# Performance work log

Measured on AMD Instinct MI355X. Metric: run time of the kernel, lower is better.

## Reference

```python
import jax, jax.numpy as jnp
import numpy as np

NUM_HEADS = 16

def setup_inputs() -> dict:
    key = jax.random.key(0)
    ks = jax.random.split(key, 6)
    b, t, d = 2, 2048, 1024
    s = 0.02
    return {
        "x": jax.random.normal(ks[0], (b, t, d), jnp.float32),
        "Wq": jax.random.normal(ks[1], (d, d), jnp.float32) * s,
        "Wk": jax.random.normal(ks[2], (d, d), jnp.float32) * s,
        "Wv": jax.random.normal(ks[3], (d, d), jnp.float32) * s,
        "Wo": jax.random.normal(ks[4], (d, d), jnp.float32) * s,
        "bo": jnp.zeros((d,), jnp.float32),
    }

def reference(x, Wq, Wk, Wv, Wo, bo):
    b, t, d = x.shape
    h = NUM_HEADS
    hd = d // h  # head_dim = d_out / num_heads
    # torch nn.Linear: y = x @ W.T (qkv_bias=False)
    def split_heads(y):
        return y.reshape(b, t, h, hd).transpose(0, 2, 1, 3)  # [b,h,t,hd]
    q = split_heads(x @ Wq.T)
    k = split_heads(x @ Wk.T)
    v = split_heads(x @ Wv.T)
    scale = 1.0 / jnp.sqrt(jnp.asarray(hd, x.dtype))
    # NOTE: original forward computes but never applies the causal mask or dropout
    scores = jnp.einsum('bhqd,bhkd->bhqk', q, k) * scale
    attn = jax.nn.softmax(scores, axis=-1)
    ctx = jnp.einsum('bhqk,bhkd->bhqd', attn, v)
    ctx = ctx.transpose(0, 2, 1, 3).reshape(b, t, d)
    return ctx @ Wo.T + bo
```

## Files before the change

### kernel.cpp

```cpp
#include <hip/hip_runtime.h>
#include <hip/hip_bf16.h>
#include <math.h>
#include <stdint.h>
#include <string.h>

#define TSEQ 2048
#define DMODEL 1024
#define NH 16
#define HD 64
#define BROWS 4096
#define BH 32

typedef __attribute__((ext_vector_type(8))) short short8;
typedef __attribute__((ext_vector_type(4))) float floatx4;
typedef __attribute__((ext_vector_type(16))) float floatx16;

#define MFMA16 __builtin_amdgcn_mfma_f32_16x16x32_bf16
#define MFMA32 __builtin_amdgcn_mfma_f32_32x32x16_bf16
#define SWZ8(r, q) ((((q) ^ ((r) & 7)) * 8))

#define QSCALE 0.18033688011112042f

__device__ __forceinline__ unsigned short bf16_rne(float f) {
    uint32_t u = __float_as_uint(f);
    u += 0x7FFFu + ((u >> 16) & 1u);
    return (unsigned short)(u >> 16);
}

__device__ __forceinline__ uint32_t pack_bf16x2(float a, float b) {
    __hip_bfloat162 h = __float22bfloat162_rn(float2{a, b});
    uint32_t r;
    memcpy(&r, &h, 4);
    return r;
}

__device__ __forceinline__ void split_bf16(float f, short& hi, short& lo) {
    uint32_t u = __float_as_uint(f);
    hi = (short)(u >> 16);
    float hif = __uint_as_float(u & 0xFFFF0000u);
    lo = (short)bf16_rne(f - hif);
}

__device__ __forceinline__ void async16(const void* g, void* l) {
    __builtin_amdgcn_global_load_lds(
        (__attribute__((address_space(1))) const uint32_t*)g,
        (__attribute__((address_space(3))) uint32_t*)l, 16, 0, 0);
}

struct PackArgs {
    const float4* x;
    ushort4* xb;
    const float4* w[3];
    ushort4* wb[3];
    const float4* wo;
    ushort4* woh;
    ushort4* wol;
};
__global__ __launch_bounds__(256) void pack_all(PackArgs a) {
    const int y = blockIdx.y;
    const int base = blockIdx.x * 256 + threadIdx.x;
    if (y == 0) {
#pragma unroll
        for (int it = 0; it < 4; ++it) {
            int i = base + it * 262144;
            float4 f = a.x[i];
            a.xb[i] = make_ushort4(bf16_rne(f.x), bf16_rne(f.y),
                                   bf16_rne(f.z), bf16_rne(f.w));
        }
    } else if (y <= 3) {
        int w = y - 1;
        float4 f = a.w[w][base];
        a.wb[w][base] = make_ushort4(bf16_rne(f.x), bf16_rne(f.y),
                                     bf16_rne(f.z), bf16_rne(f.w));
    } else {
        float4 f = a.wo[base];
        short h0, l0, h1, l1, h2, l2, h3, l3;
        split_bf16(f.x, h0, l0); split_bf16(f.y, h1, l1);
        split_bf16(f.z, h2, l2); split_bf16(f.w, h3, l3);
        a.woh[base] = make_ushort4(h0, h1, h2, h3);
        a.wol[base] = make_ushort4(l0, l1, l2, l3);
    }
}

__global__ __launch_bounds__(256) void gemm_qkv(
    const short* __restrict__ Xb,
    const short* __restrict__ Bq, const short* __restrict__ Bk,
    const short* __restrict__ Bv,
    short* __restrict__ Qo, short* __restrict__ Ko, short* __restrict__ Vo) {
    __shared__ short sA[128 * 64];
    __shared__ short sB[128 * 64];
    const int K = DMODEL;

    const int tid = threadIdx.x;
    const int lane = tid & 63, wave = tid >> 6;
    const int quad = lane >> 4, col = lane & 15;
    const int m0 = blockIdx.y * 128, n0 = blockIdx.x * 128;
    const int which = n0 >> 10;
    const int nn0 = n0 & 1023;
    const int wm = wave >> 1, wn = wave & 1;

    const short* B = (which == 0) ? Bq : (which == 1) ? Bk : Bv;
    const short* Asrc = Xb + (size_t)m0 * K;
    const short* Bsrc = B + (size_t)nn0 * K;

    const int srow = lane >> 3;
    const int soff = (((lane & 7) ^ srow) * 8);

    floatx4 acc[4][4] = {};

    for (int k0 = 0; k0 < K; k0 += 64) {
        __syncthreads();
#pragma unroll
        for (int j = 0; j < 8; ++j) {
            int idx = wave * 8 + j;
            int sub = idx & 15;
            const short* s = (idx < 16) ? Asrc : Bsrc;
            short* d = (idx < 16) ? sA : sB;
            async16(s + (size_t)(sub * 8 + srow) * K + k0 + soff, d + sub * 512);
        }
        __syncthreads();

#pragma unroll
        for (int s2 = 0; s2 < 2; ++s2) {
            short8 a_b[4], b_b[4];
#pragma unroll
            for (int mi = 0; mi < 4; ++mi) {
                int r = wm * 64 + mi * 16 + col;
                a_b[mi] = *(const short8*)&sA[r * 64 + SWZ8(r, s2 * 4 + quad)];
            }
#pragma unroll
            for (int ni = 0; ni < 4; ++ni) {
                int r = wn * 64 + ni * 16 + col;
                b_b[ni] = *(const short8*)&sB[r * 64 + SWZ8(r, s2 * 4 + quad)];
            }
            if (which == 2) {
#pragma unroll
                for (int mi = 0; mi < 4; ++mi)
#pragma unroll
                    for (int ni = 0; ni < 4; ++ni)
                        acc[mi][ni] = MFMA16(a_b[mi], b_b[ni], acc[mi][ni], 0, 0, 0);
            } else {
#pragma unroll
                for (int mi = 0; mi < 4; ++mi)
#pragma unroll
                    for (int ni = 0; ni < 4; ++ni)
                        acc[mi][ni] = MFMA16(b_b[ni], a_b[mi], acc[mi][ni], 0, 0, 0);
            }
        }
    }

    const int mb = m0 + wm * 64;
    const int nlb = nn0 + wn * 64;
    if (which == 2) {
#pragma unroll
        for (int ni = 0; ni < 4; ++ni) {
            int n = nlb + ni * 16 + col;
            int h = n >> 6, hd = n & 63;
#pragma unroll
            for (int mi = 0; mi < 4; ++mi) {
                int m4 = mb + mi * 16 + quad * 4;
                int b = m4 >> 11, t0 = m4 & 2047;
                int sw = (t0 & 0x33) | ((t0 & 4) << 1) | ((t0 & 8) >> 1);
                int tsw = (t0 & ~63) | ((((sw >> 3) ^ (hd & 7)) << 3) | (sw & 7));
                size_t row = ((size_t)(b * NH + h) * HD + hd) * TSEQ;
                *(ushort4*)&Vo[row + tsw] =
                    make_ushort4(bf16_rne(acc[mi][ni][0]), bf16_rne(acc[mi][ni][1]),
                                 bf16_rne(acc[mi][ni][2]), bf16_rne(acc[mi][ni][3]));
            }
        }
    } else {
        short* O = (which == 0) ? Qo : Ko;
        const float sc = (which == 0) ? QSCALE : 1.0f;
#pragma unroll
        for (int mi = 0; mi < 4; ++mi) {
            int m = mb + mi * 16 + col;
            int b = m >> 11, t = m & 2047;
#pragma unroll
            for (int ni = 0; ni < 4; ++ni) {
                int n = nlb + ni * 16 + quad * 4;
                int h = n >> 6, hd = n & 63;
                int hds = (which == 1) ? ((((hd >> 3) ^ (t & 7)) << 3) | (hd & 7)) : hd;
                size_t idx = ((size_t)(b * NH + h) * TSEQ + t) * HD + hds;
                *(ushort4*)&O[idx] =
                    make_ushort4(bf16_rne(acc[mi][ni][0] * sc), bf16_rne(acc[mi][ni][1] * sc),
                                 bf16_rne(acc[mi][ni][2] * sc), bf16_rne(acc[mi][ni][3] * sc));
            }
        }
    }
}

#define ATTN_COMPUTE(DB)                                                        \
    {                                                                           \
        floatx16 s[4] = {};                                                     \
        __builtin_amdgcn_s_setprio(1);                                          \
        _Pragma("unroll")                                                       \
        for (int u = 0; u < 2; ++u)                                             \
            _Pragma("unroll")                                                   \
            for (int mm = 0; mm < 2; ++mm)                                      \
                _Pragma("unroll")                                               \
                for (int ks = 0; ks < 4; ++ks) {                                \
                    short8 kf = *(const short8*)(kB[ks] + (DB) * 8192 + u * 4096 + mm * 2048); \
                    s[u * 2 + mm] = MFMA32(kf, qf[ks], s[u * 2 + mm], 0, 0, 0); \
                }                                                               \
        __builtin_amdgcn_s_setprio(0);                                          \
        _Pragma("unroll")                                                       \
        for (int m = 0; m < 4; ++m) {                                           \
            float p[16];                                                        \
            _Pragma("unroll")                                                   \
            for (int r = 0; r < 16; ++r) {                                      \
                p[r] = __builtin_amdgcn_exp2f(s[m][r]);                         \
                lv[r & 3] += p[r];                                              \
            }                                                                   \
            _Pragma("unroll")                                                   \
            for (int c = 0; c < 2; ++c) {                                       \
                union { short8 v; uint32_t w[4]; } pf;                          \
                pf.w[0] = pack_bf16x2(p[8 * c + 0], p[8 * c + 1]);              \
                pf.w[1] = pack_bf16x2(p[8 * c + 2], p[8 * c + 3]);              \
                pf.w[2] = pack_bf16x2(p[8 * c + 4], p[8 * c + 5]);              \
                pf.w[3] = pack_bf16x2(p[8 * c + 6], p[8 * c + 7]);              \
                const int t = m * 2 + c, uu = t >> 2, tt = t & 3;               \
                __builtin_amdgcn_s_setprio(1);                                  \
                _Pragma("unroll")                                               \
                for (int mi = 0; mi < 2; ++mi) {                                \
                    short8 vf = *(const short8*)(vB[tt] + (DB) * 8192 + uu * 4096 + mi * 2048); \
                    O2[mi] = MFMA32(vf, pf.v, O2[mi], 0, 0, 0);                 \
                }                                                               \
                __builtin_amdgcn_s_setprio(0);                                  \
            }                                                                   \
        }                                                                       \
    }

#define STAGE(LB)                                                               \
    {                                                                           \
        _Pragma("unroll")                                                       \
        for (int j = 0; j < 8; ++j)                                             \
            async16(gb + (size_t)j * gstride, (LB) + j * 512);                  \
        gb += ktstep;                                                           \
    }

__global__ __launch_bounds__(256, 2) void attn_bf16(
    const short* __restrict__ Qb, const short* __restrict__ Kb,
    const short* __restrict__ Vb, short* __restrict__ Cb) {
    __shared__ short sK[2][2][64 * 64];
    __shared__ short sV[2][2][64 * 64];

    const int tid = threadIdx.x;
    const int lane = tid & 63, wave = tid >> 6;
    const int q5 = lane & 31, hh = lane >> 5, l7 = lane & 7;
    const int qt = blockIdx.x, bh = blockIdx.y;
    const size_t bhoff = (size_t)bh * TSEQ * HD;

    const size_t qrow = (size_t)(qt * 128 + wave * 32 + q5) * HD;
    short8 qf[4];
#pragma unroll
    for (int ks = 0; ks < 4; ++ks)
        qf[ks] = *(const short8*)&Qb[bhoff + qrow + ks * 16 + hh * 8];

    const int srow = lane >> 3, schunk = (lane & 7) * 8;
    const int isV = wave >> 1, tl = wave & 1;
    const short* gb;
    size_t gstride, ktstep;
    if (!isV) {
        gb = Kb + bhoff + (size_t)(tl * 64 + srow) * HD + schunk;
        gstride = (size_t)8 * HD;
        ktstep = (size_t)128 * HD;
    } else {
        gb = Vb + bhoff + (size_t)srow * TSEQ + tl * 64 + schunk;
        gstride = (size_t)8 * TSEQ;
        ktstep = 128;
    }
    short* lb0 = isV ? sV[0][tl] : sK[0][tl];
    short* lb1 = isV ? sV[1][tl] : sK[1][tl];

    const short* kB[4];
    const short* vB[4];
#pragma unroll
    for (int w = 0; w < 4; ++w) {
        kB[w] = &sK[0][0][q5 * 64 + (((2 * w + hh) ^ l7) * 8)];
        vB[w] = &sV[0][0][q5 * 64 + (((2 * w + hh) ^ l7) * 8)];
    }

    floatx4 lv = {};
    floatx16 O2[2] = {};

    STAGE(lb0);

    for (int kt2 = 0; kt2 < 8; ++kt2) {
        STAGE(lb1);
        asm volatile("s_waitcnt vmcnt(8)" ::: "memory");
        __builtin_amdgcn_s_barrier();
        ATTN_COMPUTE(0);
        __builtin_amdgcn_s_barrier();

        if (kt2 < 7) {
            STAGE(lb0);
            asm volatile("s_waitcnt vmcnt(8)" ::: "memory");
        } else {
            asm volatile("s_waitcnt vmcnt(0)" ::: "memory");
        }
        __builtin_amdgcn_s_barrier();
        ATTN_COMPUTE(1);
        __builtin_amdgcn_s_barrier();
    }

    float l_r = (lv[0] + lv[1]) + (lv[2] + lv[3]);
    l_r += __shfl_xor(l_r, 32);
    const float inv = 1.0f / l_r;

    const int b = bh >> 4, h = bh & 15;
    const int trow = qt * 128 + wave * 32 + q5;
    const size_t obase = (size_t)(b * TSEQ + trow) * DMODEL + h * 64;
#pragma unroll
    for (int mi = 0; mi < 2; ++mi)
#pragma unroll
        for (int g = 0; g < 4; ++g) {
            uint2 pk;
            pk.x = pack_bf16x2(O2[mi][4 * g + 0] * inv, O2[mi][4 * g + 1] * inv);
            pk.y = pack_bf16x2(O2[mi][4 * g + 2] * inv, O2[mi][4 * g + 3] * inv);
            *(uint2*)&Cb[obase + mi * 32 + g * 8 + hh * 4] = pk;
        }
}

__global__ __launch_bounds__(256) void gemm_out(
    const short* __restrict__ Ab,
    const short* __restrict__ Bh, const short* __restrict__ Bl,
    const float* __restrict__ bias, float* __restrict__ Of) {
    __shared__ short sA[128 * 64];
    __shared__ short sBh[64 * 64];
    __shared__ short sBl[64 * 64];
    const int K = DMODEL, N = DMODEL;

    const int tid = threadIdx.x;
    const int lane = tid & 63, wave = tid >> 6;
    const int quad = lane >> 4, col = lane & 15;
    const int m0 = blockIdx.y * 128, n0 = blockIdx.x * 64;
    const int wm = wave >> 1, wn = wave & 1;

    const short* Asrc = Ab + (size_t)m0 * K;
    const short* Bhsrc = Bh + (size_t)n0 * K;
    const short* Blsrc = Bl + (size_t)n0 * K;
    const int srow = lane >> 3;
    const int soff = (((lane & 7) ^ srow) * 8);

    floatx4 acc[4][2] = {};

    for (int k0 = 0; k0 < K; k0 += 64) {
        __syncthreads();
#pragma unroll
        for (int j = 0; j < 8; ++j) {
            int idx = wave * 8 + j;
            int buf = (idx < 16) ? 0 : (idx < 24) ? 1 : 2;
            int sub = (buf == 0) ? idx : (buf == 1) ? idx - 16 : idx - 24;
            const short* s = (buf == 0) ? Asrc : (buf == 1) ? Bhsrc : Blsrc;
            short* d = (buf == 0) ? sA : (buf == 1) ? sBh : sBl;
            async16(s + (size_t)(sub * 8 + srow) * K + k0 + soff, d + sub * 512);
        }
        __syncthreads();

#pragma unroll
        for (int s2 = 0; s2 < 2; ++s2) {
            short8 a_b[4], b_h[2], b_l[2];
#pragma unroll
            for (int mi = 0; mi < 4; ++mi) {
                int r = wm * 64 + mi * 16 + col;
                a_b[mi] = *(const short8*)&sA[r * 64 + SWZ8(r, s2 * 4 + quad)];
            }
#pragma unroll
            for (int ni = 0; ni < 2; ++ni) {
                int r = wn * 32 + ni * 16 + col;
                b_h[ni] = *(const short8*)&sBh[r * 64 + SWZ8(r, s2 * 4 + quad)];
                b_l[ni] = *(const short8*)&sBl[r * 64 + SWZ8(r, s2 * 4 + quad)];
            }
#pragma unroll
            for (int mi = 0; mi < 4; ++mi)
#pragma unroll
                for (int ni = 0; ni < 2; ++ni) {
                    acc[mi][ni] = MFMA16(b_h[ni], a_b[mi], acc[mi][ni], 0, 0, 0);
                    acc[mi][ni] = MFMA16(b_l[ni], a_b[mi], acc[mi][ni], 0, 0, 0);
                }
        }
    }

    const int mb = m0 + wm * 64, nb = n0 + wn * 32;
#pragma unroll
    for (int mi = 0; mi < 4; ++mi) {
        int m = mb + mi * 16 + col;
#pragma unroll
        for (int ni = 0; ni < 2; ++ni) {
            int n = nb + ni * 16 + quad * 4;
            float4 bv = *(const float4*)&bias[n];
            float4 o = make_float4(acc[mi][ni][0] + bv.x, acc[mi][ni][1] + bv.y,
                                   acc[mi][ni][2] + bv.z, acc[mi][ni][3] + bv.w);
            *(float4*)&Of[(size_t)m * N + n] = o;
        }
    }
}

extern "C" void kernel_launch(void* const* d_in, const int* in_sizes, int n_in,
                              void* d_out, int out_size, void* d_ws, size_t ws_size,
                              hipStream_t stream) {
    const float* x  = (const float*)d_in[0];
    const float* Wq = (const float*)d_in[1];
    const float* Wk = (const float*)d_in[2];
    const float* Wv = (const float*)d_in[3];
    const float* Wo = (const float*)d_in[4];
    const float* bo = (const float*)d_in[5];
    float* out = (float*)d_out;

    const size_t NX = (size_t)BROWS * DMODEL;
    const size_t NW = (size_t)DMODEL * DMODEL;
    short* p = (short*)d_ws;
    short *xb = p;
    short *wqb = xb + NX;
    short *wkb = wqb + NW;
    short *wvb = wkb + NW;
    short *woh = wvb + NW; short *wol = woh + NW;
    short *qb = wol + NW;
    short *kb = qb + NX;
    short *vb = kb + NX;
    short *cb = vb + NX;

    PackArgs pa;
    pa.x = (const float4*)x; pa.xb = (ushort4*)xb;
    pa.w[0] = (const float4*)Wq; pa.wb[0] = (ushort4*)wqb;
    pa.w[1] = (const float4*)Wk; pa.wb[1] = (ushort4*)wkb;
    pa.w[2] = (const float4*)Wv; pa.wb[2] = (ushort4*)wvb;
    pa.wo = (const float4*)Wo; pa.woh = (ushort4*)woh; pa.wol = (ushort4*)wol;
    pack_all<<<dim3(1024, 5), dim3(256), 0, stream>>>(pa);

    gemm_qkv<<<dim3(3 * DMODEL / 128, BROWS / 128), dim3(256), 0, stream>>>(
        xb, wqb, wkb, wvb, qb, kb, vb);

    attn_bf16<<<dim3(TSEQ / 128, BH), dim3(256), 0, stream>>>(qb, kb, vb, cb);

    gemm_out<<<dim3(DMODEL / 64, BROWS / 128), dim3(256), 0, stream>>>(cb, woh, wol, bo, out);
}
```

Baseline: 192.8 us.

## Split attention KV sequence across two wave groups with LDS reduction

The attention kernel now runs 512 threads per block: two groups of four waves each take half of the key/value sequence for the same 128 query rows. Each group stages 64-key chunks into its own LDS buffers, and at the end the second group writes its partial O and row sums to shared memory for the first group to combine and normalise. This doubles the waves working on each query tile and halves the per-wave serial KV loop, aiming for more latency hiding. In exchange it adds a final LDS exchange and extra barriers, and needs more per-CU resources for the bigger blocks.

```diff
diff --git a/kernel.cpp b/kernel.cpp
--- a/kernel.cpp
+++ b/kernel.cpp
@@ -189,26 +189,24 @@
     }
 }
 
-#define ATTN_COMPUTE(DB)                                                        \
+#define ATTN_CHUNK(DB)                                                          \
     {                                                                           \
-        floatx16 s[4] = {};                                                     \
+        floatx16 s2[2] = {};                                                    \
         __builtin_amdgcn_s_setprio(1);                                          \
         _Pragma("unroll")                                                       \
-        for (int u = 0; u < 2; ++u)                                             \
+        for (int mm = 0; mm < 2; ++mm)                                          \
             _Pragma("unroll")                                                   \
-            for (int mm = 0; mm < 2; ++mm)                                      \
-                _Pragma("unroll")                                               \
-                for (int ks = 0; ks < 4; ++ks) {                                \
-                    short8 kf = *(const short8*)(kB[ks] + (DB) * 8192 + u * 4096 + mm * 2048); \
-                    s[u * 2 + mm] = MFMA32(kf, qf[ks], s[u * 2 + mm], 0, 0, 0); \
-                }                                                               \
+            for (int ks = 0; ks < 4; ++ks) {                                    \
+                short8 kf = *(const short8*)(kBp[ks] + (DB) * 4096 + mm * 2048);\
+                s2[mm] = MFMA32(kf, qf[ks], s2[mm], 0, 0, 0);                   \
+            }                                                                   \
         __builtin_amdgcn_s_setprio(0);                                          \
         _Pragma("unroll")                                                       \
-        for (int m = 0; m < 4; ++m) {                                           \
+        for (int mm = 0; mm < 2; ++mm) {                                        \
             float p[16];                                                        \
             _Pragma("unroll")                                                   \
             for (int r = 0; r < 16; ++r) {                                      \
-                p[r] = __builtin_amdgcn_exp2f(s[m][r]);                         \
+                p[r] = __builtin_amdgcn_exp2f(s2[mm][r]);                       \
                 lv[r & 3] += p[r];                                              \
             }                                                                   \
             _Pragma("unroll")                                                   \
@@ -218,11 +216,11 @@
                 pf.w[1] = pack_bf16x2(p[8 * c + 2], p[8 * c + 3]);              \
                 pf.w[2] = pack_bf16x2(p[8 * c + 4], p[8 * c + 5]);              \
                 pf.w[3] = pack_bf16x2(p[8 * c + 6], p[8 * c + 7]);              \
-                const int t = m * 2 + c, uu = t >> 2, tt = t & 3;               \
+                const int tt = mm * 2 + c;                                      \
                 __builtin_amdgcn_s_setprio(1);                                  \
                 _Pragma("unroll")                                               \
                 for (int mi = 0; mi < 2; ++mi) {                                \
-                    short8 vf = *(const short8*)(vB[tt] + (DB) * 8192 + uu * 4096 + mi * 2048); \
+                    short8 vf = *(const short8*)(vBp[tt] + (DB) * 4096 + mi * 2048); \
                     O2[mi] = MFMA32(vf, pf.v, O2[mi], 0, 0, 0);                 \
                 }                                                               \
                 __builtin_amdgcn_s_setprio(0);                                  \
@@ -232,52 +230,55 @@
 
 #define STAGE(LB)                                                               \
     {                                                                           \
-        _Pragma("unroll")                                                       \
-        for (int j = 0; j < 8; ++j)                                             \
-            async16(gb + (size_t)j * gstride, (LB) + j * 512);                  \
-        gb += ktstep;                                                           \
-    }
-
-__global__ __launch_bounds__(256, 2) void attn_bf16(
+        async16(gb + 0 * gj, (LB) + 0 * 512);                                   \
+        async16(gb + 1 * gj, (LB) + 1 * 512);                                   \
+        async16(gb + 2 * gj, (LB) + 2 * 512);                                   \
+        async16(gb + 3 * gj, (LB) + 3 * 512);                                   \
+        gb += cstep;                                                            \
+    }
+
+__global__ __launch_bounds__(512, 4) void attn_bf16(
     const short* __restrict__ Qb, const short* __restrict__ Kb,
     const short* __restrict__ Vb, short* __restrict__ Cb) {
-    __shared__ short sK[2][2][64 * 64];
-    __shared__ short sV[2][2][64 * 64];
+    __shared__ short sK[2][2][4096];
+    __shared__ short sV[2][2][4096];
 
     const int tid = threadIdx.x;
     const int lane = tid & 63, wave = tid >> 6;
     const int q5 = lane & 31, hh = lane >> 5, l7 = lane & 7;
+    const int qg = wave & 3;
+    const int st = wave >> 2;
     const int qt = blockIdx.x, bh = blockIdx.y;
     const size_t bhoff = (size_t)bh * TSEQ * HD;
 
-    const size_t qrow = (size_t)(qt * 128 + wave * 32 + q5) * HD;
+    const size_t qrow = (size_t)(qt * 128 + qg * 32 + q5) * HD;
     short8 qf[4];
 #pragma unroll
     for (int ks = 0; ks < 4; ++ks)
         qf[ks] = *(const short8*)&Qb[bhoff + qrow + ks * 16 + hh * 8];
 
     const int srow = lane >> 3, schunk = (lane & 7) * 8;
-    const int isV = wave >> 1, tl = wave & 1;
+    const int isV = qg >> 1, half = qg & 1;
     const short* gb;
-    size_t gstride, ktstep;
+    size_t gj, cstep;
     if (!isV) {
-        gb = Kb + bhoff + (size_t)(tl * 64 + srow) * HD + schunk;
-        gstride = (size_t)8 * HD;
-        ktstep = (size_t)128 * HD;
+        gb = Kb + bhoff + (size_t)(st * 1024 + half * 32 + srow) * HD + schunk;
+        gj = (size_t)8 * HD;
+        cstep = (size_t)64 * HD;
     } else {
-        gb = Vb + bhoff + (size_t)srow * TSEQ + tl * 64 + schunk;
-        gstride = (size_t)8 * TSEQ;
-        ktstep = 128;
-    }
-    short* lb0 = isV ? sV[0][tl] : sK[0][tl];
-    short* lb1 = isV ? sV[1][tl] : sK[1][tl];
-
-    const short* kB[4];
-    const short* vB[4];
+        gb = Vb + bhoff + (size_t)(half * 32 + srow) * TSEQ + st * 1024 + schunk;
+        gj = (size_t)8 * TSEQ;
+        cstep = 64;
+    }
+    short (*dst)[4096] = isV ? sV[st] : sK[st];
+    short* lb0 = dst[0] + half * 2048;
+    short* lb1 = dst[1] + half * 2048;
+
+    const short *kBp[4], *vBp[4];
 #pragma unroll
     for (int w = 0; w < 4; ++w) {
-        kB[w] = &sK[0][0][q5 * 64 + (((2 * w + hh) ^ l7) * 8)];
-        vB[w] = &sV[0][0][q5 * 64 + (((2 * w + hh) ^ l7) * 8)];
+        kBp[w] = &sK[st][0][q5 * 64 + (((2 * w + hh) ^ l7) * 8)];
+        vBp[w] = &sV[st][0][q5 * 64 + (((2 * w + hh) ^ l7) * 8)];
     }
 
     floatx4 lv = {};
@@ -285,40 +286,66 @@
 
     STAGE(lb0);
 
-    for (int kt2 = 0; kt2 < 8; ++kt2) {
+    for (int c2 = 0; c2 < 8; ++c2) {
         STAGE(lb1);
-        asm volatile("s_waitcnt vmcnt(8)" ::: "memory");
+        asm volatile("s_waitcnt vmcnt(4)" ::: "memory");
         __builtin_amdgcn_s_barrier();
-        ATTN_COMPUTE(0);
+        ATTN_CHUNK(0);
         __builtin_amdgcn_s_barrier();
 
-        if (kt2 < 7) {
+        if (c2 < 7) {
             STAGE(lb0);
-            asm volatile("s_waitcnt vmcnt(8)" ::: "memory");
+            asm volatile("s_waitcnt vmcnt(4)" ::: "memory");
         } else {
             asm volatile("s_waitcnt vmcnt(0)" ::: "memory");
         }
         __builtin_amdgcn_s_barrier();
-        ATTN_COMPUTE(1);
+        ATTN_CHUNK(1);
         __builtin_amdgcn_s_barrier();
     }
 
-    float l_r = (lv[0] + lv[1]) + (lv[2] + lv[3]);
-    l_r += __shfl_xor(l_r, 32);
-    const float inv = 1.0f / l_r;
-
-    const int b = bh >> 4, h = bh & 15;
-    const int trow = qt * 128 + wave * 32 + q5;
-    const size_t obase = (size_t)(b * TSEQ + trow) * DMODEL + h * 64;
-#pragma unroll
-    for (int mi = 0; mi < 2; ++mi)
-#pragma unroll
-        for (int g = 0; g < 4; ++g) {
+    float lp = (lv[0] + lv[1]) + (lv[2] + lv[3]);
+    float* xch = (float*)&sK[0][0][0];
+    float* xl  = (float*)&sV[0][0][0];
+    __syncthreads();
+    if (st == 1) {
+#pragma unroll
+        for (int j = 0; j < 8; ++j) {
+            float4 v = make_float4(O2[j >> 2][(j & 3) * 4 + 0],
+                                   O2[j >> 2][(j & 3) * 4 + 1],
+                                   O2[j >> 2][(j & 3) * 4 + 2],
+                                   O2[j >> 2][(j & 3) * 4 + 3]);
+            *(float4*)&xch[qg * 2048 + lane * 32 + ((j ^ l7) * 4)] = v;
+        }
+        xl[qg * 64 + lane] = lp;
+    }
+    __syncthreads();
+    if (st == 0) {
+        lp += xl[qg * 64 + lane];
+        lp += __shfl_xor(lp, 32);
+        const float inv = 1.0f / lp;
+
+        const int b = bh >> 4, h = bh & 15;
+        const int trow = qt * 128 + qg * 32 + q5;
+        const size_t obase = (size_t)(b * TSEQ + trow) * DMODEL + h * 64;
+#pragma unroll
+        for (int j = 0; j < 8; j += 2) {
+            float4 oa = *(const float4*)&xch[qg * 2048 + lane * 32 + ((j ^ l7) * 4)];
+            float4 ob = *(const float4*)&xch[qg * 2048 + lane * 32 + (((j + 1) ^ l7) * 4)];
             uint2 pk;
-            pk.x = pack_bf16x2(O2[mi][4 * g + 0] * inv, O2[mi][4 * g + 1] * inv);
-            pk.y = pack_bf16x2(O2[mi][4 * g + 2] * inv, O2[mi][4 * g + 3] * inv);
-            *(uint2*)&Cb[obase + mi * 32 + g * 8 + hh * 4] = pk;
-        }
+            pk.x = pack_bf16x2((O2[j >> 2][(j & 3) * 4 + 0] + oa.x) * inv,
+                               (O2[j >> 2][(j & 3) * 4 + 1] + oa.y) * inv);
+            pk.y = pack_bf16x2((O2[j >> 2][(j & 3) * 4 + 2] + oa.z) * inv,
+                               (O2[j >> 2][(j & 3) * 4 + 3] + oa.w) * inv);
+            uint2 pk2;
+            pk2.x = pack_bf16x2((O2[(j + 1) >> 2][((j + 1) & 3) * 4 + 0] + ob.x) * inv,
+                                (O2[(j + 1) >> 2][((j + 1) & 3) * 4 + 1] + ob.y) * inv);
+            pk2.y = pack_bf16x2((O2[(j + 1) >> 2][((j + 1) & 3) * 4 + 2] + ob.z) * inv,
+                                (O2[(j + 1) >> 2][((j + 1) & 3) * 4 + 3] + ob.w) * inv);
+            *(uint2*)&Cb[obase + (j >> 2) * 32 + (j & 3) * 8 + hh * 4] = pk;
+            *(uint2*)&Cb[obase + ((j + 1) >> 2) * 32 + ((j + 1) & 3) * 8 + hh * 4] = pk2;
+        }
+    }
 }
 
 __global__ __launch_bounds__(256) void gemm_out(
@@ -431,7 +458,7 @@
     gemm_qkv<<<dim3(3 * DMODEL / 128, BROWS / 128), dim3(256), 0, stream>>>(
         xb, wqb, wkb, wvb, qb, kb, vb);
 
-    attn_bf16<<<dim3(TSEQ / 128, BH), dim3(256), 0, stream>>>(qb, kb, vb, cb);
+    attn_bf16<<<dim3(TSEQ / 128, BH), dim3(512), 0, stream>>>(qb, kb, vb, cb);
 
     gemm_out<<<dim3(DMODEL / 64, BROWS / 128), dim3(256), 0, stream>>>(cb, woh, wol, bo, out);
 }
```

Result: slower. 202.6 us (+5.1%).
